# Kernel tuning notes

Measured on AMD Instinct MI355X. Metric: run time of the kernel, lower is better.

Reference implementation:

```python
import jax, jax.numpy as jnp
import numpy as np

N_NODES = 100000
NEG_SLOPE = 0.2
EPS = 1e-16


def gat_conv(x, src, dst, W, a_src, a_dst, bias, heads, out_dim, concat):
    # x: [N, F]; src/dst: [Etot] (self loops already appended)
    N = x.shape[0]
    h = (x @ W).reshape(N, heads, out_dim)          # [N, H, D]
    alpha_src = jnp.einsum('nhd,hd->nh', h, a_src)  # [N, H]
    alpha_dst = jnp.einsum('nhd,hd->nh', h, a_dst)  # [N, H]
    e = alpha_src[src] + alpha_dst[dst]             # [E, H]
    e = jnp.where(e > 0, e, NEG_SLOPE * e)          # leaky_relu
    # segment softmax over incoming edges of each dst node
    m = jax.ops.segment_max(e, dst, num_segments=N)
    e = jnp.exp(e - m[dst])
    s = jax.ops.segment_sum(e, dst, num_segments=N)
    alpha = e / (s[dst] + EPS)                      # [E, H]
    msg = h[src] * alpha[:, :, None]                # [E, H, D]
    out = jax.ops.segment_sum(msg, dst, num_segments=N)  # [N, H, D]
    if concat:
        out = out.reshape(N, heads * out_dim)
    else:
        out = out.mean(axis=1)
    return out + bias


def setup_inputs() -> dict:
    key = jax.random.key(0)
    ks = jax.random.split(key, 10)
    F_in, H1, D1 = 256, 8, 8
    D2 = 256 // 2  # hidden_features // 2
    x = jax.random.normal(ks[0], (N_NODES, F_in), dtype=jnp.float32)
    edge_index = jax.random.randint(ks[1], (2, 1600000), 0, N_NODES, dtype=jnp.int64)
    sc1 = 1.0 / np.sqrt(F_in)
    sc2 = 1.0 / np.sqrt(H1 * D1)
    return {
        'x': x,
        'edge_index': edge_index,
        'W1': jax.random.normal(ks[2], (F_in, H1 * D1), dtype=jnp.float32) * sc1,
        'a_src1': jax.random.normal(ks[3], (H1, D1), dtype=jnp.float32) * 0.1,
        'a_dst1': jax.random.normal(ks[4], (H1, D1), dtype=jnp.float32) * 0.1,
        'b1': jnp.zeros((H1 * D1,), dtype=jnp.float32),
        'W2': jax.random.normal(ks[5], (H1 * D1, D2), dtype=jnp.float32) * sc2,
        'a_src2': jax.random.normal(ks[6], (1, D2), dtype=jnp.float32) * 0.1,
        'a_dst2': jax.random.normal(ks[7], (1, D2), dtype=jnp.float32) * 0.1,
        'b2': jnp.zeros((D2,), dtype=jnp.float32),
    }


def reference(x, edge_index, W1, a_src1, a_dst1, b1, W2, a_src2, a_dst2, b2):
    # GAT.encode in eval mode (dropout p=0.6 disabled)
    N = x.shape[0]
    loop = jnp.arange(N, dtype=edge_index.dtype)
    src = jnp.concatenate([edge_index[0], loop])  # PyG add_self_loops
    dst = jnp.concatenate([edge_index[1], loop])
    h = gat_conv(x, src, dst, W1, a_src1, a_dst1, b1, heads=8, out_dim=8, concat=True)
    h = jax.nn.elu(h)
    z = gat_conv(h, src, dst, W2, a_src2, a_dst2, b2, heads=1, out_dim=128, concat=False)
    return z
```

## Files before the change

### kernel.cpp

```cpp
#include <hip/hip_runtime.h>
#include <hip/hip_bf16.h>
#include <cstdint>

#define H1 8
#define C1 64
#define D2 128
#define FIN 256
#define NEG 0.2f
#define EPSS 1e-16f
#define CH 1024
#define NPW2 8
#define NPB2 32
#define XPAD 264
#define XH 136
#define HP 68
#define NPBIN 128
#define TILEB 4096
#define MAXD1 128
#define MAXD2 256

template<typename T> __device__ __forceinline__ float toF(T v);
template<> __device__ __forceinline__ float toF<float>(float v) { return v; }
template<> __device__ __forceinline__ float toF<__hip_bfloat16>(__hip_bfloat16 v) { return __bfloat162float(v); }
template<typename T> __device__ __forceinline__ T fromF(float v);
template<> __device__ __forceinline__ float fromF<float>(float v) { return v; }
template<> __device__ __forceinline__ __hip_bfloat16 fromF<__hip_bfloat16>(float v) { return __float2bfloat16(v); }

__device__ __forceinline__ float bcast_lane(float v, int lane) {
    return __int_as_float(__builtin_amdgcn_readlane(__float_as_int(v), lane));
}

__device__ __forceinline__ unsigned pk_bf16(float lo, float hi) {
    unsigned a = (unsigned)__bfloat16_as_ushort(__float2bfloat16(lo));
    unsigned b = (unsigned)__bfloat16_as_ushort(__float2bfloat16(hi));
    return a | (b << 16);
}

typedef __attribute__((ext_vector_type(8))) short bf16x8;
typedef __attribute__((ext_vector_type(4))) float f32x4;

__device__ __forceinline__ void chain_upd(float ev, float hv,
                                          float& m, float& s, float& a)
{
    float mn = fmaxf(m, ev);
    float sc = __expf(m - mn);
    float p  = __expf(ev - mn);
    s = fmaf(s, sc, p);
    a = fmaf(a, sc, p * hv);
    m = mn;
}

__global__ __launch_bounds__(256) void k_wcvt(const float* __restrict__ W1,
    unsigned short* __restrict__ Wb)
{
    int t = blockIdx.x * 256 + threadIdx.x;
    int c = t >> 7, kp = t & 127;
    if (c < C1) {
        float f0 = W1[(2 * kp) * C1 + c];
        float f1 = W1[(2 * kp + 1) * C1 + c];
        *reinterpret_cast<unsigned*>(&Wb[c * XPAD + 2 * kp]) = pk_bf16(f0, f1);
    }
}

template<typename T>
__global__ __launch_bounds__(256) void k_gemm1(const float* __restrict__ x,
    const unsigned short* __restrict__ Wb, const float* __restrict__ a_src1,
    const float* __restrict__ a_dst1, T* __restrict__ h1,
    float* __restrict__ asrc1, float* __restrict__ adst1, int N)
{
    __shared__ alignas(16) unsigned short Xs[64 * XH];
    __shared__ alignas(16) unsigned short Wt[64 * XH];
    int tid = threadIdx.x;
    int wave = tid >> 6, lane = tid & 63;
    int nodeBase = blockIdx.x * 64;
    int m = lane & 15, kg = lane >> 4;
    int arow = wave * 16 + m;

    f32x4 acc[4];
    #pragma unroll
    for (int t = 0; t < 4; ++t) acc[t] = (f32x4){0.f, 0.f, 0.f, 0.f};

    #pragma unroll
    for (int kh = 0; kh < 2; ++kh) {
        for (int i = tid; i < 1024; i += 256) {
            int c = i >> 4, ch = i & 15;
            *reinterpret_cast<uint4*>(&Wt[c * XH + ch * 8]) =
                *reinterpret_cast<const uint4*>(&Wb[c * XPAD + kh * 128 + ch * 8]);
        }
        for (int i = tid; i < 2048; i += 256) {
            int r = i >> 5, q = i & 31;
            int n = nodeBase + r;
            float4 v = (n < N) ? reinterpret_cast<const float4*>(x)[(size_t)n * 64 + kh * 32 + q]
                               : make_float4(0.f, 0.f, 0.f, 0.f);
            *reinterpret_cast<uint2*>(&Xs[r * XH + q * 4]) =
                make_uint2(pk_bf16(v.x, v.y), pk_bf16(v.z, v.w));
        }
        __syncthreads();
        #pragma unroll
        for (int ks = 0; ks < 4; ++ks) {
            int k0 = ks * 32 + kg * 8;
            bf16x8 a = *reinterpret_cast<const bf16x8*>(&Xs[arow * XH + k0]);
            #pragma unroll
            for (int t = 0; t < 4; ++t) {
                bf16x8 b = *reinterpret_cast<const bf16x8*>(&Wt[(t * 16 + m) * XH + k0]);
                acc[t] = __builtin_amdgcn_mfma_f32_16x16x32_bf16(a, b, acc[t], 0, 0, 0);
            }
        }
        __syncthreads();
    }

    float* Hs = reinterpret_cast<float*>(Xs);
    int crow = (lane >> 4) * 4;
    #pragma unroll
    for (int t = 0; t < 4; ++t)
        #pragma unroll
        for (int r = 0; r < 4; ++r)
            Hs[(wave * 16 + crow + r) * HP + t * 16 + m] = acc[t][r];
    __syncthreads();

    float as_l = a_src1[lane], ad_l = a_dst1[lane];
    int n0 = nodeBase + wave * 16;
    #pragma unroll
    for (int i = 0; i < 16; ++i) {
        int n = n0 + i;
        if (n >= N) break;
        float hv = Hs[(wave * 16 + i) * HP + lane];
        h1[(size_t)n * C1 + lane] = fromF<T>(hv);
        float vs = hv * as_l, vd = hv * ad_l;
        #pragma unroll
        for (int off = 1; off < 8; off <<= 1) {
            vs += __shfl_xor(vs, off);
            vd += __shfl_xor(vd, off);
        }
        if ((lane & 7) == 0) {
            asrc1[n * H1 + (lane >> 3)] = vs;
            adst1[n * H1 + (lane >> 3)] = vd;
        }
    }
}

__global__ __launch_bounds__(128) void k_wvec(const float* __restrict__ W2,
    const float* __restrict__ a_src2, const float* __restrict__ a_dst2,
    float* __restrict__ wsrc, float* __restrict__ wdst)
{
    int t = threadIdx.x;
    int k = t & 63;
    const float* a = (t < 64) ? a_src2 : a_dst2;
    float s = 0.f;
    for (int c = 0; c < D2; ++c) s = fmaf(W2[k * D2 + c], a[c], s);
    if (t < 64) wsrc[k] = s; else wdst[k] = s;
}

__global__ __launch_bounds__(256) void k_binhist(const int* __restrict__ ei, int E, int N,
    int nbins, int* __restrict__ binCnt)
{
    __shared__ int lcnt[1024];
    int tot = E + N;
    int t0 = blockIdx.x * TILEB;
    int cnt = min(TILEB, tot - t0);
    for (int i = threadIdx.x; i < nbins; i += 256) lcnt[i] = 0;
    __syncthreads();
    for (int i = threadIdx.x; i < cnt; i += 256) {
        int e = t0 + i;
        int dst = (e < E) ? ei[(size_t)E + e] : (e - E);
        atomicAdd(&lcnt[dst >> 7], 1);
    }
    __syncthreads();
    for (int i = threadIdx.x; i < nbins; i += 256)
        if (lcnt[i]) atomicAdd(&binCnt[i], lcnt[i]);
}

__global__ __launch_bounds__(256) void k_binscan(const int* __restrict__ binCnt,
    int* __restrict__ binOff, int* __restrict__ binCur, int nbins)
{
    __shared__ int wtot[4];
    int t = threadIdx.x, lane = t & 63, wave = t >> 6;
    int v[4];
    #pragma unroll
    for (int j = 0; j < 4; ++j) {
        int idx = t * 4 + j;
        v[j] = (idx < nbins) ? binCnt[idx] : 0;
    }
    int s = v[0] + v[1] + v[2] + v[3];
    int incl = s;
    #pragma unroll
    for (int off = 1; off < 64; off <<= 1) {
        int tt = __shfl_up(incl, off);
        if (lane >= off) incl += tt;
    }
    if (lane == 63) wtot[wave] = incl;
    __syncthreads();
    int woff = 0;
    #pragma unroll
    for (int w = 0; w < 4; ++w) if (w < wave) woff += wtot[w];
    int run = woff + incl - s;
    #pragma unroll
    for (int j = 0; j < 4; ++j) {
        int idx = t * 4 + j;
        if (idx < nbins) { binOff[idx] = run; binCur[idx] = run; }
        run += v[j];
    }
    if (t == 255) binOff[nbins] = woff + incl;
}

__global__ __launch_bounds__(256) void k_bin(const int* __restrict__ ei, int E, int N,
    int nbins, int* __restrict__ binCur, int* __restrict__ binned)
{
    __shared__ int recs[TILEB];
    __shared__ unsigned short bns[TILEB];
    __shared__ int lcnt[1024];
    __shared__ int lbase[1024];
    int tot = E + N;
    int t0 = blockIdx.x * TILEB;
    int cnt = min(TILEB, tot - t0);
    for (int i = threadIdx.x; i < nbins; i += 256) lcnt[i] = 0;
    __syncthreads();
    for (int i = threadIdx.x; i < cnt; i += 256) {
        int e = t0 + i;
        int src, dst;
        if (e < E) { src = ei[e]; dst = ei[(size_t)E + e]; }
        else       { src = e - E; dst = src; }
        int b = dst >> 7;
        recs[i] = src | ((dst & 127) << 17);
        bns[i] = (unsigned short)b;
        atomicAdd(&lcnt[b], 1);
    }
    __syncthreads();
    for (int i = threadIdx.x; i < nbins; i += 256) {
        int c = lcnt[i];
        if (c) lbase[i] = atomicAdd(&binCur[i], c);
        lcnt[i] = 0;
    }
    __syncthreads();
    for (int i = threadIdx.x; i < cnt; i += 256) {
        int b = bns[i];
        int lp = atomicAdd(&lcnt[b], 1);
        binned[lbase[b] + lp] = recs[i];
    }
}

__global__ __launch_bounds__(256) void k_binptr(const int* __restrict__ binOff,
    const int* __restrict__ binned, int* __restrict__ ptr,
    int* __restrict__ edge_src, int N, int nbins)
{
    __shared__ int cnt[NPBIN];
    __shared__ int cur[NPBIN];
    __shared__ int w0tot;
    int b = blockIdx.x, t = threadIdx.x;
    int s0 = binOff[b], s1 = binOff[b + 1];
    if (t < NPBIN) cnt[t] = 0;
    __syncthreads();
    for (int i = s0 + t; i < s1; i += 256)
        atomicAdd(&cnt[binned[i] >> 17], 1);
    __syncthreads();
    int v = 0, incl = 0;
    if (t < NPBIN) {
        int lane = t & 63;
        v = cnt[t];
        incl = v;
        #pragma unroll
        for (int off = 1; off < 64; off <<= 1) {
            int tt = __shfl_up(incl, off);
            if (lane >= off) incl += tt;
        }
        if (t == 63) w0tot = incl;
    }
    __syncthreads();
    if (t < NPBIN) {
        int base = s0 + ((t >= 64) ? w0tot : 0);
        int excl = base + incl - v;
        int node = b * NPBIN + t;
        if (node < N) ptr[node] = excl;
        cur[t] = excl;
    }
    if (b == nbins - 1 && t == 0) ptr[N] = s1;
    __syncthreads();
    for (int i = s0 + t; i < s1; i += 256) {
        int rec = binned[i];
        int p = atomicAdd(&cur[rec >> 17], 1);
        edge_src[p] = rec & 0x1FFFF;
    }
}

__global__ void k_count(const int* __restrict__ ei, int E, int N,
                        int* __restrict__ deg)
{
    int tot = E + N;
    for (int e = blockIdx.x * blockDim.x + threadIdx.x; e < tot;
         e += gridDim.x * blockDim.x) {
        int dst = (e < E) ? ei[(size_t)E + e] : (e - E);
        atomicAdd(&deg[dst], 1);
    }
}

__global__ void k_scatter(const int* __restrict__ ei, int E, int N,
                          int* __restrict__ cursor, int* __restrict__ edge_src)
{
    int tot = E + N;
    for (int e = blockIdx.x * blockDim.x + threadIdx.x; e < tot;
         e += gridDim.x * blockDim.x) {
        int src, dst;
        if (e < E) { src = ei[e]; dst = ei[(size_t)E + e]; }
        else       { src = e - E; dst = e - E; }
        int pos = atomicAdd(&cursor[dst], 1);
        edge_src[pos] = src;
    }
}

__global__ __launch_bounds__(256) void k_scanA(const int* __restrict__ deg,
    int* __restrict__ ptr, int* __restrict__ chunkSum)
{
    __shared__ int wtot[4];
    int b = blockIdx.x, t = threadIdx.x;
    int lane = t & 63, wave = t >> 6;
    int4 v = reinterpret_cast<const int4*>(deg + (size_t)b * CH)[t];
    int s = v.x + v.y + v.z + v.w;
    int incl = s;
    #pragma unroll
    for (int off = 1; off < 64; off <<= 1) {
        int tt = __shfl_up(incl, off);
        if (lane >= off) incl += tt;
    }
    if (lane == 63) wtot[wave] = incl;
    __syncthreads();
    int woff = 0;
    #pragma unroll
    for (int w = 0; w < 4; ++w) if (w < wave) woff += wtot[w];
    int excl = woff + incl - s;
    int i0 = b * CH + t * 4;
    ptr[i0 + 0] = excl;
    ptr[i0 + 1] = excl + v.x;
    ptr[i0 + 2] = excl + v.x + v.y;
    ptr[i0 + 3] = excl + v.x + v.y + v.z;
    if (t == 255) chunkSum[b] = woff + incl;
}

__global__ void k_scanB(const int* __restrict__ chunkSum, int* __restrict__ chunkOff,
                        int NB, int* __restrict__ ptrN)
{
    if (threadIdx.x == 0) {
        int c = 0;
        for (int b = 0; b < NB; ++b) { chunkOff[b] = c; c += chunkSum[b]; }
        *ptrN = c;
    }
}

__global__ __launch_bounds__(256) void k_scanC(int* __restrict__ ptr,
    int* __restrict__ cursor, const int* __restrict__ chunkOff, int N)
{
    int b = blockIdx.x;
    int off = chunkOff[b];
    int i0 = b * CH + threadIdx.x * 4;
    #pragma unroll
    for (int k = 0; k < 4; ++k) {
        int i = i0 + k;
        if (i < N) { int v = ptr[i] + off; ptr[i] = v; cursor[i] = v; }
    }
}

template<typename T>
__global__ __launch_bounds__(256) void k_agg1(const int* __restrict__ ptr,
    const int* __restrict__ edge_src, const T* __restrict__ h1,
    const float* __restrict__ asrc1, const float* __restrict__ adst1,
    const float* __restrict__ b1, const float* __restrict__ wsrc,
    const float* __restrict__ wdst, T* __restrict__ hmid,
    float* __restrict__ asrc2, float* __restrict__ adst2, int N)
{
    __shared__ float S1[4 * MAXD1 * H1];
    int wave = threadIdx.x >> 6, lane = threadIdx.x & 63;
    float* st = S1 + wave * (MAXD1 * H1);
    int n = blockIdx.x * 4 + wave;
    if (n >= N) return;
    int start = ptr[n], end = ptr[n + 1];
    int deg = end - start;
    int h = lane >> 3;
    float o;

    if (deg <= MAXD1) {
        int e_loc = lane >> 3, hh = lane & 7;
        float adsth = adst1[n * H1 + hh];
        float mloc = -1e30f;
        for (int eb = start, base = 0; eb < end; eb += 8, base += 64) {
            int e = eb + e_loc;
            float ev = -1e30f;
            if (e < end) {
                int s = edge_src[e];
                ev = asrc1[s * H1 + hh] + adsth;
                ev = ev > 0.f ? ev : NEG * ev;
                st[base + lane] = ev;
            }
            mloc = fmaxf(mloc, ev);
        }
        mloc = fmaxf(mloc, __shfl_xor(mloc, 8));
        mloc = fmaxf(mloc, __shfl_xor(mloc, 16));
        mloc = fmaxf(mloc, __shfl_xor(mloc, 32));
        __builtin_amdgcn_wave_barrier();
        float sloc = 0.f;
        for (int eb = start, base = 0; eb < end; eb += 8, base += 64) {
            if (eb + e_loc < end) {
                float p = __expf(st[base + lane] - mloc);
                st[base + lane] = p;
                sloc += p;
            }
        }
        sloc += __shfl_xor(sloc, 8);
        sloc += __shfl_xor(sloc, 16);
        sloc += __shfl_xor(sloc, 32);
        float inv = 1.f / (sloc + EPSS);
        __builtin_amdgcn_wave_barrier();
        float inv_c = __shfl(inv, h);

        float a0 = 0.f, a1 = 0.f, a2 = 0.f, a3 = 0.f;
        float a4 = 0.f, a5 = 0.f, a6 = 0.f, a7 = 0.f;
        int e = start;
        for (; e + 8 <= end; e += 8) {
            int r = e - start;
            int i0 = edge_src[e + 0]; int i1 = edge_src[e + 1];
            int i2 = edge_src[e + 2]; int i3 = edge_src[e + 3];
            int i4 = edge_src[e + 4]; int i5 = edge_src[e + 5];
            int i6 = edge_src[e + 6]; int i7 = edge_src[e + 7];
            float w0 = st[(r + 0) * H1 + h]; float w1 = st[(r + 1) * H1 + h];
            float w2 = st[(r + 2) * H1 + h]; float w3 = st[(r + 3) * H1 + h];
            float w4 = st[(r + 4) * H1 + h]; float w5 = st[(r + 5) * H1 + h];
            float w6 = st[(r + 6) * H1 + h]; float w7 = st[(r + 7) * H1 + h];
            a0 = fmaf(w0, toF(h1[((size_t)(unsigned)i0 << 6) + lane]), a0);
            a1 = fmaf(w1, toF(h1[((size_t)(unsigned)i1 << 6) + lane]), a1);
            a2 = fmaf(w2, toF(h1[((size_t)(unsigned)i2 << 6) + lane]), a2);
            a3 = fmaf(w3, toF(h1[((size_t)(unsigned)i3 << 6) + lane]), a3);
            a4 = fmaf(w4, toF(h1[((size_t)(unsigned)i4 << 6) + lane]), a4);
            a5 = fmaf(w5, toF(h1[((size_t)(unsigned)i5 << 6) + lane]), a5);
            a6 = fmaf(w6, toF(h1[((size_t)(unsigned)i6 << 6) + lane]), a6);
            a7 = fmaf(w7, toF(h1[((size_t)(unsigned)i7 << 6) + lane]), a7);
        }
        for (; e < end; ++e) {
            int s = edge_src[e];
            a0 = fmaf(st[(e - start) * H1 + h],
                      toF(h1[((size_t)(unsigned)s << 6) + lane]), a0);
        }
        float acc = ((a0 + a1) + (a2 + a3)) + ((a4 + a5) + (a6 + a7));
        o = acc * inv_c;
    } else {
        float adst = adst1[n * H1 + h];
        float m[8], ss[8], aa[8];
        #pragma unroll
        for (int j = 0; j < 8; ++j) { m[j] = -1e30f; ss[j] = 0.f; aa[j] = 0.f; }
        int e = start;
        for (; e + 8 <= end; e += 8) {
            int idx[8];
            #pragma unroll
            for (int j = 0; j < 8; ++j) idx[j] = edge_src[e + j];
            #pragma unroll
            for (int j = 0; j < 8; ++j) {
                float t = asrc1[idx[j] * H1 + h] + adst;
                t = t > 0.f ? t : NEG * t;
                chain_upd(t, toF(h1[((size_t)(unsigned)idx[j] << 6) + lane]),
                          m[j], ss[j], aa[j]);
            }
        }
        for (; e < end; ++e) {
            int s = edge_src[e];
            float t = asrc1[s * H1 + h] + adst;
            t = t > 0.f ? t : NEG * t;
            chain_upd(t, toF(h1[((size_t)(unsigned)s << 6) + lane]), m[0], ss[0], aa[0]);
        }
        float M = fmaxf(fmaxf(fmaxf(m[0], m[1]), fmaxf(m[2], m[3])),
                        fmaxf(fmaxf(m[4], m[5]), fmaxf(m[6], m[7])));
        float sum = 0.f, acc = 0.f;
        #pragma unroll
        for (int j = 0; j < 8; ++j) {
            float sc = __expf(m[j] - M);
            sum = fmaf(ss[j], sc, sum);
            acc = fmaf(aa[j], sc, acc);
        }
        o = acc / (sum + EPSS);
    }

    o = o + b1[lane];
    o = o > 0.f ? o : (expf(o) - 1.f);
    hmid[(size_t)n * C1 + lane] = fromF<T>(o);
    float vs = o * wsrc[lane];
    float vd = o * wdst[lane];
    #pragma unroll
    for (int off = 1; off < 64; off <<= 1) {
        vs += __shfl_xor(vs, off);
        vd += __shfl_xor(vd, off);
    }
    if (lane == 0) { asrc2[n] = vs; adst2[n] = vd; }
}

template<typename T>
__global__ __launch_bounds__(256) void k_agg2(const int* __restrict__ ptr,
    const int* __restrict__ edge_src, const T* __restrict__ hmid,
    const float* __restrict__ asrc2, const float* __restrict__ adst2,
    T* __restrict__ aggv_out, int N)
{
    __shared__ float S2[4 * MAXD2];
    int wave = threadIdx.x >> 6, lane = threadIdx.x & 63;
    float* st = S2 + wave * MAXD2;
    int n = blockIdx.x * 4 + wave;
    if (n >= N) return;
    int start = ptr[n], end = ptr[n + 1];
    int deg = end - start;
    float adst = adst2[n];
    float aggv;

    if (deg <= MAXD2) {
        float mloc = -1e30f;
        for (int e = start + lane; e < end; e += 64) {
            int s = edge_src[e];
            float ev = asrc2[s] + adst;
            ev = ev > 0.f ? ev : NEG * ev;
            st[e - start] = ev;
            mloc = fmaxf(mloc, ev);
        }
        #pragma unroll
        for (int off = 1; off < 64; off <<= 1)
            mloc = fmaxf(mloc, __shfl_xor(mloc, off));
        __builtin_amdgcn_wave_barrier();
        float sloc = 0.f;
        for (int e = start + lane; e < end; e += 64) {
            float p = __expf(st[e - start] - mloc);
            st[e - start] = p;
            sloc += p;
        }
        #pragma unroll
        for (int off = 1; off < 64; off <<= 1)
            sloc += __shfl_xor(sloc, off);
        float inv = 1.f / (sloc + EPSS);
        __builtin_amdgcn_wave_barrier();

        float a0 = 0.f, a1 = 0.f, a2 = 0.f, a3 = 0.f;
        float a4 = 0.f, a5 = 0.f, a6 = 0.f, a7 = 0.f;
        int e = start;
        for (; e + 8 <= end; e += 8) {
            int r = e - start;
            int i0 = edge_src[e + 0]; int i1 = edge_src[e + 1];
            int i2 = edge_src[e + 2]; int i3 = edge_src[e + 3];
            int i4 = edge_src[e + 4]; int i5 = edge_src[e + 5];
            int i6 = edge_src[e + 6]; int i7 = edge_src[e + 7];
            a0 = fmaf(st[r + 0], toF(hmid[((size_t)(unsigned)i0 << 6) + lane]), a0);
            a1 = fmaf(st[r + 1], toF(hmid[((size_t)(unsigned)i1 << 6) + lane]), a1);
            a2 = fmaf(st[r + 2], toF(hmid[((size_t)(unsigned)i2 << 6) + lane]), a2);
            a3 = fmaf(st[r + 3], toF(hmid[((size_t)(unsigned)i3 << 6) + lane]), a3);
            a4 = fmaf(st[r + 4], toF(hmid[((size_t)(unsigned)i4 << 6) + lane]), a4);
            a5 = fmaf(st[r + 5], toF(hmid[((size_t)(unsigned)i5 << 6) + lane]), a5);
            a6 = fmaf(st[r + 6], toF(hmid[((size_t)(unsigned)i6 << 6) + lane]), a6);
            a7 = fmaf(st[r + 7], toF(hmid[((size_t)(unsigned)i7 << 6) + lane]), a7);
        }
        for (; e < end; ++e) {
            int s = edge_src[e];
            a0 = fmaf(st[e - start], toF(hmid[((size_t)(unsigned)s << 6) + lane]), a0);
        }
        float acc = ((a0 + a1) + (a2 + a3)) + ((a4 + a5) + (a6 + a7));
        aggv = acc * inv;
    } else {
        float m[8], ss[8], aa[8];
        #pragma unroll
        for (int j = 0; j < 8; ++j) { m[j] = -1e30f; ss[j] = 0.f; aa[j] = 0.f; }
        int e = start;
        for (; e + 8 <= end; e += 8) {
            int idx[8];
            #pragma unroll
            for (int j = 0; j < 8; ++j) idx[j] = edge_src[e + j];
            #pragma unroll
            for (int j = 0; j < 8; ++j) {
                float t = asrc2[idx[j]] + adst;
                t = t > 0.f ? t : NEG * t;
                chain_upd(t, toF(hmid[((size_t)(unsigned)idx[j] << 6) + lane]),
                          m[j], ss[j], aa[j]);
            }
        }
        for (; e < end; ++e) {
            int s = edge_src[e];
            float t = asrc2[s] + adst;
            t = t > 0.f ? t : NEG * t;
            chain_upd(t, toF(hmid[((size_t)(unsigned)s << 6) + lane]), m[0], ss[0], aa[0]);
        }
        float M = fmaxf(fmaxf(fmaxf(m[0], m[1]), fmaxf(m[2], m[3])),
                        fmaxf(fmaxf(m[4], m[5]), fmaxf(m[6], m[7])));
        float sum = 0.f, acc = 0.f;
        #pragma unroll
        for (int j = 0; j < 8; ++j) {
            float sc = __expf(m[j] - M);
            sum = fmaf(ss[j], sc, sum);
            acc = fmaf(aa[j], sc, acc);
        }
        aggv = acc / (sum + EPSS);
    }
    aggv_out[(size_t)n * C1 + lane] = fromF<T>(aggv);
}

template<typename T>
__global__ __launch_bounds__(256) void k_gemm2(const T* __restrict__ aggv,
    const float* __restrict__ W2, const float* __restrict__ b2,
    float* __restrict__ out, int N)
{
    __shared__ float Ws[C1 * D2];
    for (int i = threadIdx.x; i < C1 * D2 / 4; i += 256)
        reinterpret_cast<float4*>(Ws)[i] = reinterpret_cast<const float4*>(W2)[i];

    int wave = threadIdx.x >> 6, lane = threadIdx.x & 63;
    int n0 = blockIdx.x * NPB2 + wave * NPW2;

    float av[NPW2];
    #pragma unroll
    for (int j = 0; j < NPW2; ++j) {
        int n = n0 + j;
        av[j] = (n < N) ? toF(aggv[(size_t)n * C1 + lane]) : 0.f;
    }
    __syncthreads();

    float acc0[NPW2], acc1[NPW2];
    #pragma unroll
    for (int j = 0; j < NPW2; ++j) { acc0[j] = 0.f; acc1[j] = 0.f; }

    #pragma unroll 4
    for (int k = 0; k < 64; ++k) {
        float w0 = Ws[k * D2 + lane];
        float w1 = Ws[k * D2 + 64 + lane];
        #pragma unroll
        for (int j = 0; j < NPW2; ++j) {
            float xk = bcast_lane(av[j], k);
            acc0[j] = fmaf(xk, w0, acc0[j]);
            acc1[j] = fmaf(xk, w1, acc1[j]);
        }
    }

    float bb0 = b2[lane], bb1 = b2[64 + lane];
    #pragma unroll
    for (int j = 0; j < NPW2; ++j) {
        int n = n0 + j;
        if (n >= N) continue;
        out[(size_t)n * D2 + lane]      = acc0[j] + bb0;
        out[(size_t)n * D2 + 64 + lane] = acc1[j] + bb1;
    }
}

extern "C" void kernel_launch(void* const* d_in, const int* in_sizes, int n_in,
                              void* d_out, int out_size, void* d_ws, size_t ws_size,
                              hipStream_t stream)
{
    const float* x      = (const float*)d_in[0];
    const int*   ei     = (const int*)d_in[1];
    const float* W1     = (const float*)d_in[2];
    const float* a_src1 = (const float*)d_in[3];
    const float* a_dst1 = (const float*)d_in[4];
    const float* b1     = (const float*)d_in[5];
    const float* W2     = (const float*)d_in[6];
    const float* a_src2 = (const float*)d_in[7];
    const float* a_dst2 = (const float*)d_in[8];
    const float* b2     = (const float*)d_in[9];
    float* out = (float*)d_out;

    const int N = in_sizes[0] / FIN;
    const int E = in_sizes[1] / 2;
    const int Etot = E + N;
    const int NB = (N + CH - 1) / CH;
    const size_t NP = (size_t)NB * CH;

    const size_t common =
        ((size_t)N * H1 * 4 + 255 & ~(size_t)255) * 2 +
        (((size_t)N * 4 + 255) & ~(size_t)255) * 2 +
        512 +
        (((size_t)NP * 4 + 255) & ~(size_t)255) * 2 +
        (((size_t)(NP + 1) * 4 + 255) & ~(size_t)255) +
        (((size_t)NB * 4 + 255) & ~(size_t)255) * 2 +
        (((size_t)Etot * 4 + 255) & ~(size_t)255) +
        (64 * XPAD * 2 + 256) +
        4096;
    const bool f32path = ws_size >= common + 2 * ((size_t)N * C1 * 4 + 256);

    char* ws = (char*)d_ws;
    size_t off = 0;
    auto alloc = [&](size_t bytes) -> void* {
        void* p = ws + off;
        off = (off + bytes + 255) & ~(size_t)255;
        return p;
    };
    const size_t es = f32path ? 4 : 2;
    void*  h1v    = alloc((size_t)N * C1 * es);
    void*  hmidv  = alloc((size_t)N * C1 * es);
    float* asrc1  = (float*)alloc((size_t)N * H1 * 4);
    float* adst1  = (float*)alloc((size_t)N * H1 * 4);
    float* asrc2  = (float*)alloc((size_t)N * 4);
    float* adst2  = (float*)alloc((size_t)N * 4);
    float* wsrc   = (float*)alloc(64 * 4);
    float* wdst   = (float*)alloc(64 * 4);
    int*   deg    = (int*)alloc(NP * 4);
    int*   ptr    = (int*)alloc((NP + 1) * 4);
    int*   cursor = (int*)alloc(NP * 4);
    int*   chunkSum = (int*)alloc((size_t)NB * 4);
    int*   chunkOff = (int*)alloc((size_t)NB * 4);
    int*   edge_src = (int*)alloc((size_t)Etot * 4);
    unsigned short* Wb = (unsigned short*)alloc(64 * XPAD * 2);

    const int nodeBlocks = (N + 3) / 4;
    const int g1Blocks = (N + 63) / 64;
    const int g2Blocks = (N + NPB2 - 1) / NPB2;

    k_wcvt<<<32, 256, 0, stream>>>(W1, Wb);

    const int nbins = (N + NPBIN - 1) / NPBIN;
    const bool binpath = (N <= (1 << 17)) &&
                         ((size_t)Etot * 4 <= (size_t)N * C1 * es);
    if (binpath) {
        int* binned = (int*)h1v;
        int* binCnt = (int*)hmidv;
        int* binOff = binCnt + 1056;
        int* binCur = binOff + 1056;
        const int binBlocks = (Etot + TILEB - 1) / TILEB;
        hipMemsetAsync(binCnt, 0, (size_t)nbins * 4, stream);
        k_binhist<<<binBlocks, 256, 0, stream>>>(ei, E, N, nbins, binCnt);
        k_binscan<<<1, 256, 0, stream>>>(binCnt, binOff, binCur, nbins);
        k_bin<<<binBlocks, 256, 0, stream>>>(ei, E, N, nbins, binCur, binned);
        k_binptr<<<nbins, 256, 0, stream>>>(binOff, binned, ptr, edge_src, N, nbins);
    } else {
        hipMemsetAsync(deg, 0, NP * 4, stream);
        k_count<<<2048, 256, 0, stream>>>(ei, E, N, deg);
        k_scanA<<<NB, 256, 0, stream>>>(deg, ptr, chunkSum);
        k_scanB<<<1, 64, 0, stream>>>(chunkSum, chunkOff, NB, ptr + N);
        k_scanC<<<NB, 256, 0, stream>>>(ptr, cursor, chunkOff, N);
        k_scatter<<<2048, 256, 0, stream>>>(ei, E, N, cursor, edge_src);
    }

    k_wvec<<<1, 128, 0, stream>>>(W2, a_src2, a_dst2, wsrc, wdst);

    if (f32path) {
        float* h1 = (float*)h1v; float* hmid = (float*)hmidv;
        k_gemm1<float><<<g1Blocks, 256, 0, stream>>>(x, Wb, a_src1, a_dst1, h1, asrc1, adst1, N);
        k_agg1<float><<<nodeBlocks, 256, 0, stream>>>(ptr, edge_src, h1, asrc1, adst1, b1,
                                                      wsrc, wdst, hmid, asrc2, adst2, N);
        float* aggv = (float*)h1v;
        k_agg2<float><<<nodeBlocks, 256, 0, stream>>>(ptr, edge_src, hmid, asrc2, adst2, aggv, N);
        k_gemm2<float><<<g2Blocks, 256, 0, stream>>>(aggv, W2, b2, out, N);
    } else {
        __hip_bfloat16* h1 = (__hip_bfloat16*)h1v; __hip_bfloat16* hmid = (__hip_bfloat16*)hmidv;
        k_gemm1<__hip_bfloat16><<<g1Blocks, 256, 0, stream>>>(x, Wb, a_src1, a_dst1, h1, asrc1, adst1, N);
        k_agg1<__hip_bfloat16><<<nodeBlocks, 256, 0, stream>>>(ptr, edge_src, h1, asrc1, adst1, b1,
                                                               wsrc, wdst, hmid, asrc2, adst2, N);
        __hip_bfloat16* aggv = (__hip_bfloat16*)h1v;
        k_agg2<__hip_bfloat16><<<nodeBlocks, 256, 0, stream>>>(ptr, edge_src, hmid, asrc2, adst2, aggv, N);
        k_gemm2<__hip_bfloat16><<<g2Blocks, 256, 0, stream>>>(aggv, W2, b2, out, N);
    }
}
```

Baseline: 344.6 us.

## Fuse layer-2 aggregation with W2 projection and shrink GEMM1 K-tile

Merges the layer-2 aggregation and output GEMM into one kernel. Each wave now multiplies its aggregated 64-vector by a bf16 copy of W2 held in shared memory and writes the final output directly, so the intermediate aggv buffer is no longer written and re-read. Separately, GEMM1 uses 64-wide K tiles over four steps instead of 128-wide over two, cutting its shared memory use and likely raising occupancy. The costs are loading 16KB of W2 into shared memory in every 4-node block, which is many tiny blocks, plus bf16 rounding of W2.

```diff
diff --git a/kernel.cpp b/kernel.cpp
--- a/kernel.cpp
+++ b/kernel.cpp
@@ -9,10 +9,8 @@
 #define NEG 0.2f
 #define EPSS 1e-16f
 #define CH 1024
-#define NPW2 8
-#define NPB2 32
 #define XPAD 264
-#define XH 136
+#define XQ 72
 #define HP 68
 #define NPBIN 128
 #define TILEB 4096
@@ -36,6 +34,11 @@
     return a | (b << 16);
 }
 
+__device__ __forceinline__ float bf16u_toF(unsigned short u) {
+    unsigned v = ((unsigned)u) << 16;
+    return __uint_as_float(v);
+}
+
 typedef __attribute__((ext_vector_type(8))) short bf16x8;
 typedef __attribute__((ext_vector_type(4))) float f32x4;
 
@@ -62,14 +65,25 @@
     }
 }
 
+__global__ __launch_bounds__(256) void k_w2cvt(const float* __restrict__ W2,
+    unsigned short* __restrict__ W2b)
+{
+    int t = blockIdx.x * 256 + threadIdx.x;
+    if (t < C1 * D2 / 2) {
+        float f0 = W2[2 * t], f1 = W2[2 * t + 1];
+        *reinterpret_cast<unsigned*>(&W2b[2 * t]) = pk_bf16(f0, f1);
+    }
+}
+
 template<typename T>
 __global__ __launch_bounds__(256) void k_gemm1(const float* __restrict__ x,
     const unsigned short* __restrict__ Wb, const float* __restrict__ a_src1,
     const float* __restrict__ a_dst1, T* __restrict__ h1,
     float* __restrict__ asrc1, float* __restrict__ adst1, int N)
 {
-    __shared__ alignas(16) unsigned short Xs[64 * XH];
-    __shared__ alignas(16) unsigned short Wt[64 * XH];
+    __shared__ alignas(16) char smem[2 * 64 * XQ * 2];
+    unsigned short* Xs = (unsigned short*)smem;
+    unsigned short* Wt = (unsigned short*)(smem + 64 * XQ * 2);
     int tid = threadIdx.x;
     int wave = tid >> 6, lane = tid & 63;
     int nodeBase = blockIdx.x * 64;
@@ -81,35 +95,35 @@
     for (int t = 0; t < 4; ++t) acc[t] = (f32x4){0.f, 0.f, 0.f, 0.f};
 
     #pragma unroll
-    for (int kh = 0; kh < 2; ++kh) {
+    for (int kh = 0; kh < 4; ++kh) {
+        for (int i = tid; i < 512; i += 256) {
+            int c = i >> 3, ch = i & 7;
+            *reinterpret_cast<uint4*>(&Wt[c * XQ + ch * 8]) =
+                *reinterpret_cast<const uint4*>(&Wb[c * XPAD + kh * 64 + ch * 8]);
+        }
         for (int i = tid; i < 1024; i += 256) {
-            int c = i >> 4, ch = i & 15;
-            *reinterpret_cast<uint4*>(&Wt[c * XH + ch * 8]) =
-                *reinterpret_cast<const uint4*>(&Wb[c * XPAD + kh * 128 + ch * 8]);
-        }
-        for (int i = tid; i < 2048; i += 256) {
-            int r = i >> 5, q = i & 31;
+            int r = i >> 4, q = i & 15;
             int n = nodeBase + r;
-            float4 v = (n < N) ? reinterpret_cast<const float4*>(x)[(size_t)n * 64 + kh * 32 + q]
+            float4 v = (n < N) ? reinterpret_cast<const float4*>(x)[(size_t)n * 64 + kh * 16 + q]
                                : make_float4(0.f, 0.f, 0.f, 0.f);
-            *reinterpret_cast<uint2*>(&Xs[r * XH + q * 4]) =
+            *reinterpret_cast<uint2*>(&Xs[r * XQ + q * 4]) =
                 make_uint2(pk_bf16(v.x, v.y), pk_bf16(v.z, v.w));
         }
         __syncthreads();
         #pragma unroll
-        for (int ks = 0; ks < 4; ++ks) {
+        for (int ks = 0; ks < 2; ++ks) {
             int k0 = ks * 32 + kg * 8;
-            bf16x8 a = *reinterpret_cast<const bf16x8*>(&Xs[arow * XH + k0]);
+            bf16x8 a = *reinterpret_cast<const bf16x8*>(&Xs[arow * XQ + k0]);
             #pragma unroll
             for (int t = 0; t < 4; ++t) {
-                bf16x8 b = *reinterpret_cast<const bf16x8*>(&Wt[(t * 16 + m) * XH + k0]);
+                bf16x8 b = *reinterpret_cast<const bf16x8*>(&Wt[(t * 16 + m) * XQ + k0]);
                 acc[t] = __builtin_amdgcn_mfma_f32_16x16x32_bf16(a, b, acc[t], 0, 0, 0);
             }
         }
         __syncthreads();
     }
 
-    float* Hs = reinterpret_cast<float*>(Xs);
+    float* Hs = reinterpret_cast<float*>(smem);
     int crow = (lane >> 4) * 4;
     #pragma unroll
     for (int t = 0; t < 4; ++t)
@@ -489,12 +503,18 @@
 }
 
 template<typename T>
-__global__ __launch_bounds__(256) void k_agg2(const int* __restrict__ ptr,
+__global__ __launch_bounds__(256) void k_agg2out(const int* __restrict__ ptr,
     const int* __restrict__ edge_src, const T* __restrict__ hmid,
     const float* __restrict__ asrc2, const float* __restrict__ adst2,
-    T* __restrict__ aggv_out, int N)
-{
+    const unsigned short* __restrict__ W2b, const float* __restrict__ b2,
+    float* __restrict__ out, int N)
+{
+    __shared__ unsigned short Ws[C1 * D2];
     __shared__ float S2[4 * MAXD2];
+    for (int i = threadIdx.x; i < C1 * D2 / 8; i += 256)
+        reinterpret_cast<uint4*>(Ws)[i] = reinterpret_cast<const uint4*>(W2b)[i];
+    __syncthreads();
+
     int wave = threadIdx.x >> 6, lane = threadIdx.x & 63;
     float* st = S2 + wave * MAXD2;
     int n = blockIdx.x * 4 + wave;
@@ -587,53 +607,18 @@
         }
         aggv = acc / (sum + EPSS);
     }
-    aggv_out[(size_t)n * C1 + lane] = fromF<T>(aggv);
-}
-
-template<typename T>
-__global__ __launch_bounds__(256) void k_gemm2(const T* __restrict__ aggv,
-    const float* __restrict__ W2, const float* __restrict__ b2,
-    float* __restrict__ out, int N)
-{
-    __shared__ float Ws[C1 * D2];
-    for (int i = threadIdx.x; i < C1 * D2 / 4; i += 256)
-        reinterpret_cast<float4*>(Ws)[i] = reinterpret_cast<const float4*>(W2)[i];
-
-    int wave = threadIdx.x >> 6, lane = threadIdx.x & 63;
-    int n0 = blockIdx.x * NPB2 + wave * NPW2;
-
-    float av[NPW2];
-    #pragma unroll
-    for (int j = 0; j < NPW2; ++j) {
-        int n = n0 + j;
-        av[j] = (n < N) ? toF(aggv[(size_t)n * C1 + lane]) : 0.f;
-    }
-    __syncthreads();
-
-    float acc0[NPW2], acc1[NPW2];
-    #pragma unroll
-    for (int j = 0; j < NPW2; ++j) { acc0[j] = 0.f; acc1[j] = 0.f; }
-
-    #pragma unroll 4
+
+    float acc0 = 0.f, acc1 = 0.f;
+    #pragma unroll
     for (int k = 0; k < 64; ++k) {
-        float w0 = Ws[k * D2 + lane];
-        float w1 = Ws[k * D2 + 64 + lane];
-        #pragma unroll
-        for (int j = 0; j < NPW2; ++j) {
-            float xk = bcast_lane(av[j], k);
-            acc0[j] = fmaf(xk, w0, acc0[j]);
-            acc1[j] = fmaf(xk, w1, acc1[j]);
-        }
-    }
-
-    float bb0 = b2[lane], bb1 = b2[64 + lane];
-    #pragma unroll
-    for (int j = 0; j < NPW2; ++j) {
-        int n = n0 + j;
-        if (n >= N) continue;
-        out[(size_t)n * D2 + lane]      = acc0[j] + bb0;
-        out[(size_t)n * D2 + 64 + lane] = acc1[j] + bb1;
-    }
+        float xk = bcast_lane(aggv, k);
+        float w0 = bf16u_toF(Ws[k * D2 + lane]);
+        float w1 = bf16u_toF(Ws[k * D2 + 64 + lane]);
+        acc0 = fmaf(xk, w0, acc0);
+        acc1 = fmaf(xk, w1, acc1);
+    }
+    out[(size_t)n * D2 + lane]      = acc0 + b2[lane];
+    out[(size_t)n * D2 + 64 + lane] = acc1 + b2[64 + lane];
 }
 
 extern "C" void kernel_launch(void* const* d_in, const int* in_sizes, int n_in,
@@ -667,6 +652,7 @@
         (((size_t)NB * 4 + 255) & ~(size_t)255) * 2 +
         (((size_t)Etot * 4 + 255) & ~(size_t)255) +
         (64 * XPAD * 2 + 256) +
+        (C1 * D2 * 2 + 256) +
         4096;
     const bool f32path = ws_size >= common + 2 * ((size_t)N * C1 * 4 + 256);
 
@@ -692,13 +678,14 @@
     int*   chunkSum = (int*)alloc((size_t)NB * 4);
     int*   chunkOff = (int*)alloc((size_t)NB * 4);
     int*   edge_src = (int*)alloc((size_t)Etot * 4);
-    unsigned short* Wb = (unsigned short*)alloc(64 * XPAD * 2);
+    unsigned short* Wb  = (unsigned short*)alloc(64 * XPAD * 2);
+    unsigned short* W2b = (unsigned short*)alloc(C1 * D2 * 2);
 
     const int nodeBlocks = (N + 3) / 4;
     const int g1Blocks = (N + 63) / 64;
-    const int g2Blocks = (N + NPB2 - 1) / NPB2;
 
     k_wcvt<<<32, 256, 0, stream>>>(W1, Wb);
+    k_w2cvt<<<16, 256, 0, stream>>>(W2, W2b);
 
     const int nbins = (N + NPBIN - 1) / NPBIN;
     const bool binpath = (N <= (1 << 17)) &&
@@ -730,16 +717,14 @@
         k_gemm1<float><<<g1Blocks, 256, 0, stream>>>(x, Wb, a_src1, a_dst1, h1, asrc1, adst1, N);
         k_agg1<float><<<nodeBlocks, 256, 0, stream>>>(ptr, edge_src, h1, asrc1, adst1, b1,
                                                       wsrc, wdst, hmid, asrc2, adst2, N);
-        float* aggv = (float*)h1v;
-        k_agg2<float><<<nodeBlocks, 256, 0, stream>>>(ptr, edge_src, hmid, asrc2, adst2, aggv, N);
-        k_gemm2<float><<<g2Blocks, 256, 0, stream>>>(aggv, W2, b2, out, N);
+        k_agg2out<float><<<nodeBlocks, 256, 0, stream>>>(ptr, edge_src, hmid, asrc2, adst2,
+                                                         W2b, b2, out, N);
     } else {
         __hip_bfloat16* h1 = (__hip_bfloat16*)h1v; __hip_bfloat16* hmid = (__hip_bfloat16*)hmidv;
         k_gemm1<__hip_bfloat16><<<g1Blocks, 256, 0, stream>>>(x, Wb, a_src1, a_dst1, h1, asrc1, adst1, N);
         k_agg1<__hip_bfloat16><<<nodeBlocks, 256, 0, stream>>>(ptr, edge_src, h1, asrc1, adst1, b1,
                                                                wsrc, wdst, hmid, asrc2, adst2, N);
-        __hip_bfloat16* aggv = (__hip_bfloat16*)h1v;
-        k_agg2<__hip_bfloat16><<<nodeBlocks, 256, 0, stream>>>(ptr, edge_src, hmid, asrc2, adst2, aggv, N);
-        k_gemm2<__hip_bfloat16><<<g2Blocks, 256, 0, stream>>>(aggv, W2, b2, out, N);
-    }
-}
+        k_agg2out<__hip_bfloat16><<<nodeBlocks, 256, 0, stream>>>(ptr, edge_src, hmid, asrc2, adst2,
+                                                                  W2b, b2, out, N);
+    }
+}
```

Measured after the change: 335.6 us. 1.03x faster.
